# Kernel optimization log

Hardware: AMD Instinct MI355X
Metric: run time of the kernel (lower is better)

The kernel has to match this reference:

```python
import jax, jax.numpy as jnp
from jax import lax
import numpy as np

B, T, I, H, OUT = 4096, 168, 4, 64, 12


def setup_inputs() -> dict:
    key = jax.random.key(0)
    ks = jax.random.split(key, 14)
    s = 0.05
    return {
        "x": jax.random.normal(ks[0], (B, T, I), dtype=jnp.float32),
        # LSTM layer 0 (PyTorch gate order: i, f, g, o)
        "Wih0": jax.random.normal(ks[1], (4 * H, I), dtype=jnp.float32) * s,
        "Whh0": jax.random.normal(ks[2], (4 * H, H), dtype=jnp.float32) * s,
        "bih0": jax.random.normal(ks[3], (4 * H,), dtype=jnp.float32) * s,
        "bhh0": jax.random.normal(ks[4], (4 * H,), dtype=jnp.float32) * s,
        # LSTM layer 1
        "Wih1": jax.random.normal(ks[5], (4 * H, H), dtype=jnp.float32) * s,
        "Whh1": jax.random.normal(ks[6], (4 * H, H), dtype=jnp.float32) * s,
        "bih1": jax.random.normal(ks[7], (4 * H,), dtype=jnp.float32) * s,
        "bhh1": jax.random.normal(ks[8], (4 * H,), dtype=jnp.float32) * s,
        # FC head: Linear(64,64) -> ReLU -> Linear(64,12)
        "W1": jax.random.normal(ks[9], (64, H), dtype=jnp.float32) * s,
        "b1": jax.random.normal(ks[10], (64,), dtype=jnp.float32) * s,
        "W2": jax.random.normal(ks[11], (OUT, 64), dtype=jnp.float32) * s,
        "b2": jax.random.normal(ks[12], (OUT,), dtype=jnp.float32) * s,
    }


def _lstm_layer(x, Wih, Whh, bih, bhh):
    # x: [B, T, in]; returns hidden sequence [B, T, H]
    Bsz = x.shape[0]
    Hd = Whh.shape[1]
    # Precompute input contribution for all timesteps: [B, T, 4H]
    xg = jnp.einsum('bti,gi->btg', x, Wih) + bih + bhh

    def step(carry, xg_t):
        h, c = carry
        g = xg_t + h @ Whh.T  # [B, 4H]
        i, f, gg, o = jnp.split(g, 4, axis=-1)
        i = jax.nn.sigmoid(i)
        f = jax.nn.sigmoid(f)
        gg = jnp.tanh(gg)
        o = jax.nn.sigmoid(o)
        c = f * c + i * gg
        h = o * jnp.tanh(c)
        return (h, c), h

    h0 = jnp.zeros((Bsz, Hd), x.dtype)
    (_, _), hs = lax.scan(step, (h0, h0), jnp.swapaxes(xg, 0, 1))  # hs: [T, B, H]
    return jnp.swapaxes(hs, 0, 1)


def reference(x, Wih0, Whh0, bih0, bhh0, Wih1, Whh1, bih1, bhh1, W1, b1, W2, b2):
    # Eval-mode forward: dropout layers are identity.
    h1 = _lstm_layer(x, Wih0, Whh0, bih0, bhh0)   # [B, T, H]
    h2 = _lstm_layer(h1, Wih1, Whh1, bih1, bhh1)  # [B, T, H]
    last = h2[:, -1, :]                            # [B, H]
    z = jax.nn.relu(last @ W1.T + b1)              # [B, 64]
    out = z @ W2.T + b2                            # [B, 12]
    return out.reshape(-1, 3, 4)
```

## Files before the change

kernel.cpp:

```cpp
#include <hip/hip_runtime.h>


typedef _Float16 h8 __attribute__((ext_vector_type(8)));
typedef _Float16 h4 __attribute__((ext_vector_type(4)));
typedef float f4 __attribute__((ext_vector_type(4)));

#define ROWB 208
#define HBUF (16 * ROWB)
#define H0_OFF 0
#define H1_OFF (2 * HBUF)
#define SMEM_TOTAL (4 * HBUF)

__device__ __forceinline__ float rcp_(float x) {
#if __has_builtin(__builtin_amdgcn_rcpf)
  return __builtin_amdgcn_rcpf(x);
#else
  return 1.f / x;
#endif
}
__device__ __forceinline__ float sigm(float x) { return rcp_(1.f + __expf(-x)); }
__device__ __forceinline__ float tanh_(float x) { return 2.f * rcp_(1.f + __expf(-2.f * x)) - 1.f; }

__device__ __forceinline__ f4 mfma16(h8 a, h8 b, f4 c) {
  return __builtin_amdgcn_mfma_f32_16x16x32_f16(a, b, c, 0, 0, 0);
}

__device__ __forceinline__ h8 load_w8(const float* __restrict__ p) {
  h8 r;
#pragma unroll
  for (int j = 0; j < 8; j++) r[j] = (_Float16)p[j];
  return r;
}

extern "C" __global__ void __launch_bounds__(512, 2)
weather_lstm_mfma(const float* __restrict__ x,
                  const float* __restrict__ Wih0, const float* __restrict__ Whh0,
                  const float* __restrict__ bih0, const float* __restrict__ bhh0,
                  const float* __restrict__ Wih1, const float* __restrict__ Whh1,
                  const float* __restrict__ bih1, const float* __restrict__ bhh1,
                  const float* __restrict__ W1, const float* __restrict__ b1,
                  const float* __restrict__ W2, const float* __restrict__ b2,
                  float* __restrict__ out)
{
  __shared__ __align__(16) unsigned char smem[SMEM_TOTAL];
  const int tid  = threadIdx.x;
  const int lane = tid & 63;
  const int w    = tid >> 6;
  const int col  = lane & 15;
  const int quad = lane >> 4;
  const int sB   = blockIdx.x * 16;

  const int g_  = col & 3;
  const int ul_ = col >> 2;
  int arow[2];
  arow[0] = g_ * 64 + w * 8 + 0 + ul_;
  arow[1] = g_ * 64 + w * 8 + 4 + ul_;

  h8 a0[2][3];
  h8 a1i[2][2];
  h8 a1h[2][2];
#pragma unroll
  for (int T = 0; T < 2; T++) {
    const int r = arow[T];
#pragma unroll
    for (int f = 0; f < 2; f++) {
      a0[T][f]  = load_w8(Whh0 + r * 64 + f * 32 + quad * 8);
      a1i[T][f] = load_w8(Wih1 + r * 64 + f * 32 + quad * 8);
      a1h[T][f] = load_w8(Whh1 + r * 64 + f * 32 + quad * 8);
    }
    h8 xw = {};
    if (quad == 0) {
#pragma unroll
      for (int j = 0; j < 4; j++) xw[j] = (_Float16)Wih0[r * 4 + j];
    }
    a0[T][2] = xw;
  }

  f4 bias0v[2], bias1v[2];
#pragma unroll
  for (int T = 0; T < 2; T++) {
#pragma unroll
    for (int reg = 0; reg < 4; reg++) {
      const int rr = reg * 64 + w * 8 + T * 4 + quad;
      bias0v[T][reg] = bih0[rr] + bhh0[rr];
      bias1v[T][reg] = bih1[rr] + bhh1[rr];
    }
  }

  for (int idx = tid; idx < SMEM_TOTAL / 4; idx += 512) ((int*)smem)[idx] = 0;
  __syncthreads();
  if (tid < 16) {
    f4 xv = *(const f4*)(x + ((size_t)(sB + tid) * 168 + 0) * 4);
    h4 xh;
#pragma unroll
    for (int j = 0; j < 4; j++) xh[j] = (_Float16)xv[j];
    *(h4*)(smem + H0_OFF + 0 * HBUF + tid * ROWB + 128) = xh;
  }
  __syncthreads();

  float c0[2] = {0.f, 0.f}, c1[2] = {0.f, 0.f};
  float hl[2] = {0.f, 0.f};
  const int bo = col * ROWB + quad * 16;

  for (int t = 0; t < 168; t++) {
    const int pb = t & 1, nb = pb ^ 1;
    unsigned char* h0p = smem + H0_OFF + pb * HBUF;
    unsigned char* h0n = smem + H0_OFF + nb * HBUF;
    unsigned char* h1p = smem + H1_OFF + pb * HBUF;
    unsigned char* h1n = smem + H1_OFF + nb * HBUF;

    if (tid < 16) {
      const int tn = (t < 167) ? t + 1 : 167;
      f4 xv = *(const f4*)(x + ((size_t)(sB + tid) * 168 + tn) * 4);
      h4 xh;
#pragma unroll
      for (int j = 0; j < 4; j++) xh[j] = (_Float16)xv[j];
      *(h4*)(h0n + tid * ROWB + 128) = xh;
    }

    h8 b0 = *(const h8*)(h0p + bo);
    h8 b1v = *(const h8*)(h0p + bo + 64);
    h8 b2v = *(const h8*)(h0p + bo + 128);

    f4 acc0 = bias0v[0], acc1 = bias0v[1];
    acc0 = mfma16(a0[0][0], b0, acc0);
    acc1 = mfma16(a0[1][0], b0, acc1);
    acc0 = mfma16(a0[0][1], b1v, acc0);
    acc1 = mfma16(a0[1][1], b1v, acc1);
    acc0 = mfma16(a0[0][2], b2v, acc0);
    acc1 = mfma16(a0[1][2], b2v, acc1);

#pragma unroll
    for (int T = 0; T < 2; T++) {
      f4 a = T ? acc1 : acc0;
      float iv = sigm(a[0]);
      float fv = sigm(a[1]);
      float gv = tanh_(a[2]);
      float ov = sigm(a[3]);
      c0[T] = fv * c0[T] + iv * gv;
      float hn = ov * tanh_(c0[T]);
      *(_Float16*)(h0n + col * ROWB + (w * 8 + T * 4 + quad) * 2) = (_Float16)hn;
    }
    __syncthreads();

    h8 p0 = *(const h8*)(h0n + bo);
    h8 p1 = *(const h8*)(h0n + bo + 64);
    h8 q0 = *(const h8*)(h1p + bo);
    h8 q1 = *(const h8*)(h1p + bo + 64);

    acc0 = bias1v[0]; acc1 = bias1v[1];
    acc0 = mfma16(a1i[0][0], p0, acc0);
    acc1 = mfma16(a1i[1][0], p0, acc1);
    acc0 = mfma16(a1i[0][1], p1, acc0);
    acc1 = mfma16(a1i[1][1], p1, acc1);
    acc0 = mfma16(a1h[0][0], q0, acc0);
    acc1 = mfma16(a1h[1][0], q0, acc1);
    acc0 = mfma16(a1h[0][1], q1, acc0);
    acc1 = mfma16(a1h[1][1], q1, acc1);

#pragma unroll
    for (int T = 0; T < 2; T++) {
      f4 a = T ? acc1 : acc0;
      float iv = sigm(a[0]);
      float fv = sigm(a[1]);
      float gv = tanh_(a[2]);
      float ov = sigm(a[3]);
      c1[T] = fv * c1[T] + iv * gv;
      float hn = ov * tanh_(c1[T]);
      hl[T] = hn;
      *(_Float16*)(h1n + col * ROWB + (w * 8 + T * 4 + quad) * 2) = (_Float16)hn;
    }
    __syncthreads();
  }

  float* fh = (float*)smem;
#pragma unroll
  for (int T = 0; T < 2; T++)
    fh[col * 64 + (w * 8 + T * 4 + quad)] = hl[T];
  __syncthreads();

  {
    const int u = tid & 63, grp = tid >> 6;
    float za0 = b1[u], za1 = b1[u];
    const float* w1r = W1 + u * 64;
    const float* f0 = fh + (grp * 2 + 0) * 64;
    const float* f1 = fh + (grp * 2 + 1) * 64;
    for (int j = 0; j < 64; j++) {
      float wv = w1r[j];
      za0 += wv * f0[j];
      za1 += wv * f1[j];
    }
    float* zl = (float*)(smem + 4096);
    zl[(grp * 2 + 0) * 64 + u] = fmaxf(za0, 0.f);
    zl[(grp * 2 + 1) * 64 + u] = fmaxf(za1, 0.f);
  }
  __syncthreads();

  if (tid < 192) {
    const float* zl = (const float*)(smem + 4096);
    const int s = tid / 12, o = tid - s * 12;
    float a = b2[o];
    for (int j = 0; j < 64; j++) a += W2[o * 64 + j] * zl[s * 64 + j];
    out[(sB + s) * 12 + o] = a;
  }
}

extern "C" void kernel_launch(void* const* d_in, const int* in_sizes, int n_in,
                              void* d_out, int out_size, void* d_ws, size_t ws_size,
                              hipStream_t stream) {
  (void)in_sizes; (void)n_in; (void)d_ws; (void)ws_size; (void)out_size;
  const float* x    = (const float*)d_in[0];
  const float* Wih0 = (const float*)d_in[1];
  const float* Whh0 = (const float*)d_in[2];
  const float* bih0 = (const float*)d_in[3];
  const float* bhh0 = (const float*)d_in[4];
  const float* Wih1 = (const float*)d_in[5];
  const float* Whh1 = (const float*)d_in[6];
  const float* bih1 = (const float*)d_in[7];
  const float* bhh1 = (const float*)d_in[8];
  const float* W1   = (const float*)d_in[9];
  const float* b1   = (const float*)d_in[10];
  const float* W2   = (const float*)d_in[11];
  const float* b2   = (const float*)d_in[12];

  weather_lstm_mfma<<<dim3(256), dim3(512), 0, stream>>>(
      x, Wih0, Whh0, bih0, bhh0, Wih1, Whh1, bih1, bhh1, W1, b1, W2, b2,
      (float*)d_out);
}
```

Measured before the change: 252.6 us.

## Prescale gate weights by log2e, hoist layer-1 recurrent MFMAs, pack h stores

Folds the log2(e) and 2·log2(e) factors into the fp16 weights and biases so the sigmoid and tanh use raw exp2 and rcp with no per-element multiply. The layer-1 recurrent MFMAs on h1(t-1) are moved ahead of the barrier so they run alongside layer 0, shortening the serial dependency chain each timestep. Gate rows are permuted so each lane owns two adjacent hidden units, letting the two fp16 h values be written as one packed 32-bit LDS store. Scaling weights before fp16 conversion slightly changes rounding.

Result: faster. 233.3 us (-7.7%).

```diff
diff --git a/kernel.cpp b/kernel.cpp
--- a/kernel.cpp
+++ b/kernel.cpp
@@ -11,36 +11,52 @@
 #define H1_OFF (2 * HBUF)
 #define SMEM_TOTAL (4 * HBUF)
 
+#define K1F 1.4426950408889634f
+#define K2F 2.8853900817779268f
+
+__device__ __forceinline__ float exp2_(float x) {
+#if __has_builtin(__builtin_amdgcn_exp2f)
+  return __builtin_amdgcn_exp2f(x);
+#else
+  float r; asm("v_exp_f32 %0, %1" : "=v"(r) : "v"(x)); return r;
+#endif
+}
 __device__ __forceinline__ float rcp_(float x) {
 #if __has_builtin(__builtin_amdgcn_rcpf)
   return __builtin_amdgcn_rcpf(x);
 #else
-  return 1.f / x;
+  float r; asm("v_rcp_f32 %0, %1" : "=v"(r) : "v"(x)); return r;
 #endif
 }
-__device__ __forceinline__ float sigm(float x) { return rcp_(1.f + __expf(-x)); }
-__device__ __forceinline__ float tanh_(float x) { return 2.f * rcp_(1.f + __expf(-2.f * x)) - 1.f; }
+__device__ __forceinline__ float sigmp(float a) { return rcp_(1.f + exp2_(-a)); }
+__device__ __forceinline__ float tanhp(float a) { return 1.f - 2.f * rcp_(exp2_(a) + 1.f); }
 
 __device__ __forceinline__ f4 mfma16(h8 a, h8 b, f4 c) {
   return __builtin_amdgcn_mfma_f32_16x16x32_f16(a, b, c, 0, 0, 0);
 }
 
-__device__ __forceinline__ h8 load_w8(const float* __restrict__ p) {
+__device__ __forceinline__ h8 load_w8s(const float* __restrict__ p, float sc) {
   h8 r;
 #pragma unroll
-  for (int j = 0; j < 8; j++) r[j] = (_Float16)p[j];
+  for (int j = 0; j < 8; j++) r[j] = (_Float16)(p[j] * sc);
   return r;
 }
 
+__device__ __forceinline__ unsigned packh2(float a, float b) {
+  unsigned lo = (unsigned)__builtin_bit_cast(unsigned short, (_Float16)a);
+  unsigned hi = (unsigned)__builtin_bit_cast(unsigned short, (_Float16)b);
+  return lo | (hi << 16);
+}
+
 extern "C" __global__ void __launch_bounds__(512, 2)
-weather_lstm_mfma(const float* __restrict__ x,
-                  const float* __restrict__ Wih0, const float* __restrict__ Whh0,
-                  const float* __restrict__ bih0, const float* __restrict__ bhh0,
-                  const float* __restrict__ Wih1, const float* __restrict__ Whh1,
-                  const float* __restrict__ bih1, const float* __restrict__ bhh1,
-                  const float* __restrict__ W1, const float* __restrict__ b1,
-                  const float* __restrict__ W2, const float* __restrict__ b2,
-                  float* __restrict__ out)
+weather_lstm_mfma3(const float* __restrict__ x,
+                   const float* __restrict__ Wih0, const float* __restrict__ Whh0,
+                   const float* __restrict__ bih0, const float* __restrict__ bhh0,
+                   const float* __restrict__ Wih1, const float* __restrict__ Whh1,
+                   const float* __restrict__ bih1, const float* __restrict__ bhh1,
+                   const float* __restrict__ W1, const float* __restrict__ b1,
+                   const float* __restrict__ W2, const float* __restrict__ b2,
+                   float* __restrict__ out)
 {
   __shared__ __align__(16) unsigned char smem[SMEM_TOTAL];
   const int tid  = threadIdx.x;
@@ -52,26 +68,25 @@
 
   const int g_  = col & 3;
   const int ul_ = col >> 2;
+  const float asc = (g_ == 2) ? K2F : K1F;
   int arow[2];
-  arow[0] = g_ * 64 + w * 8 + 0 + ul_;
-  arow[1] = g_ * 64 + w * 8 + 4 + ul_;
-
-  h8 a0[2][3];
-  h8 a1i[2][2];
-  h8 a1h[2][2];
+  arow[0] = g_ * 64 + w * 8 + 2 * ul_ + 0;
+  arow[1] = g_ * 64 + w * 8 + 2 * ul_ + 1;
+
+  h8 a0[2][3], a1i[2][2], a1h[2][2];
 #pragma unroll
   for (int T = 0; T < 2; T++) {
     const int r = arow[T];
 #pragma unroll
     for (int f = 0; f < 2; f++) {
-      a0[T][f]  = load_w8(Whh0 + r * 64 + f * 32 + quad * 8);
-      a1i[T][f] = load_w8(Wih1 + r * 64 + f * 32 + quad * 8);
-      a1h[T][f] = load_w8(Whh1 + r * 64 + f * 32 + quad * 8);
+      a0[T][f]  = load_w8s(Whh0 + r * 64 + f * 32 + quad * 8, asc);
+      a1i[T][f] = load_w8s(Wih1 + r * 64 + f * 32 + quad * 8, asc);
+      a1h[T][f] = load_w8s(Whh1 + r * 64 + f * 32 + quad * 8, asc);
     }
     h8 xw = {};
     if (quad == 0) {
 #pragma unroll
-      for (int j = 0; j < 4; j++) xw[j] = (_Float16)Wih0[r * 4 + j];
+      for (int j = 0; j < 4; j++) xw[j] = (_Float16)(Wih0[r * 4 + j] * asc);
     }
     a0[T][2] = xw;
   }
@@ -81,9 +96,10 @@
   for (int T = 0; T < 2; T++) {
 #pragma unroll
     for (int reg = 0; reg < 4; reg++) {
-      const int rr = reg * 64 + w * 8 + T * 4 + quad;
-      bias0v[T][reg] = bih0[rr] + bhh0[rr];
-      bias1v[T][reg] = bih1[rr] + bhh1[rr];
+      const int rr = reg * 64 + w * 8 + 2 * quad + T;
+      const float bs = (reg == 2) ? K2F : K1F;
+      bias0v[T][reg] = (bih0[rr] + bhh0[rr]) * bs;
+      bias1v[T][reg] = (bih1[rr] + bhh1[rr]) * bs;
     }
   }
 
@@ -101,6 +117,7 @@
   float c0[2] = {0.f, 0.f}, c1[2] = {0.f, 0.f};
   float hl[2] = {0.f, 0.f};
   const int bo = col * ROWB + quad * 16;
+  const int wo = col * ROWB + (w * 8 + 2 * quad) * 2;
 
   for (int t = 0; t < 168; t++) {
     const int pb = t & 1, nb = pb ^ 1;
@@ -118,65 +135,63 @@
       *(h4*)(h0n + tid * ROWB + 128) = xh;
     }
 
-    h8 b0 = *(const h8*)(h0p + bo);
+    h8 b0  = *(const h8*)(h0p + bo);
     h8 b1v = *(const h8*)(h0p + bo + 64);
     h8 b2v = *(const h8*)(h0p + bo + 128);
-
-    f4 acc0 = bias0v[0], acc1 = bias0v[1];
-    acc0 = mfma16(a0[0][0], b0, acc0);
-    acc1 = mfma16(a0[1][0], b0, acc1);
+    h8 q0  = *(const h8*)(h1p + bo);
+    h8 q1  = *(const h8*)(h1p + bo + 64);
+
+    f4 l1a0 = mfma16(a1h[0][0], q0, bias1v[0]);
+    f4 l1a1 = mfma16(a1h[1][0], q0, bias1v[1]);
+    l1a0 = mfma16(a1h[0][1], q1, l1a0);
+    l1a1 = mfma16(a1h[1][1], q1, l1a1);
+
+    f4 acc0 = mfma16(a0[0][0], b0, bias0v[0]);
+    f4 acc1 = mfma16(a0[1][0], b0, bias0v[1]);
     acc0 = mfma16(a0[0][1], b1v, acc0);
     acc1 = mfma16(a0[1][1], b1v, acc1);
     acc0 = mfma16(a0[0][2], b2v, acc0);
     acc1 = mfma16(a0[1][2], b2v, acc1);
 
+    float h0o[2];
 #pragma unroll
     for (int T = 0; T < 2; T++) {
       f4 a = T ? acc1 : acc0;
-      float iv = sigm(a[0]);
-      float fv = sigm(a[1]);
-      float gv = tanh_(a[2]);
-      float ov = sigm(a[3]);
+      float iv = sigmp(a[0]);
+      float fv = sigmp(a[1]);
+      float gv = tanhp(a[2]);
+      float ov = sigmp(a[3]);
       c0[T] = fv * c0[T] + iv * gv;
-      float hn = ov * tanh_(c0[T]);
-      *(_Float16*)(h0n + col * ROWB + (w * 8 + T * 4 + quad) * 2) = (_Float16)hn;
-    }
+      h0o[T] = ov * tanhp(c0[T] * K2F);
+    }
+    *(unsigned*)(h0n + wo) = packh2(h0o[0], h0o[1]);
     __syncthreads();
 
     h8 p0 = *(const h8*)(h0n + bo);
     h8 p1 = *(const h8*)(h0n + bo + 64);
-    h8 q0 = *(const h8*)(h1p + bo);
-    h8 q1 = *(const h8*)(h1p + bo + 64);
-
-    acc0 = bias1v[0]; acc1 = bias1v[1];
-    acc0 = mfma16(a1i[0][0], p0, acc0);
-    acc1 = mfma16(a1i[1][0], p0, acc1);
-    acc0 = mfma16(a1i[0][1], p1, acc0);
-    acc1 = mfma16(a1i[1][1], p1, acc1);
-    acc0 = mfma16(a1h[0][0], q0, acc0);
-    acc1 = mfma16(a1h[1][0], q0, acc1);
-    acc0 = mfma16(a1h[0][1], q1, acc0);
-    acc1 = mfma16(a1h[1][1], q1, acc1);
+    l1a0 = mfma16(a1i[0][0], p0, l1a0);
+    l1a1 = mfma16(a1i[1][0], p0, l1a1);
+    l1a0 = mfma16(a1i[0][1], p1, l1a0);
+    l1a1 = mfma16(a1i[1][1], p1, l1a1);
 
 #pragma unroll
     for (int T = 0; T < 2; T++) {
-      f4 a = T ? acc1 : acc0;
-      float iv = sigm(a[0]);
-      float fv = sigm(a[1]);
-      float gv = tanh_(a[2]);
-      float ov = sigm(a[3]);
+      f4 a = T ? l1a1 : l1a0;
+      float iv = sigmp(a[0]);
+      float fv = sigmp(a[1]);
+      float gv = tanhp(a[2]);
+      float ov = sigmp(a[3]);
       c1[T] = fv * c1[T] + iv * gv;
-      float hn = ov * tanh_(c1[T]);
-      hl[T] = hn;
-      *(_Float16*)(h1n + col * ROWB + (w * 8 + T * 4 + quad) * 2) = (_Float16)hn;
-    }
+      hl[T] = ov * tanhp(c1[T] * K2F);
+    }
+    *(unsigned*)(h1n + wo) = packh2(hl[0], hl[1]);
     __syncthreads();
   }
 
   float* fh = (float*)smem;
 #pragma unroll
   for (int T = 0; T < 2; T++)
-    fh[col * 64 + (w * 8 + T * 4 + quad)] = hl[T];
+    fh[col * 64 + (w * 8 + 2 * quad + T)] = hl[T];
   __syncthreads();
 
   {
@@ -223,7 +238,7 @@
   const float* W2   = (const float*)d_in[11];
   const float* b2   = (const float*)d_in[12];
 
-  weather_lstm_mfma<<<dim3(256), dim3(512), 0, stream>>>(
+  weather_lstm_mfma3<<<dim3(256), dim3(512), 0, stream>>>(
       x, Wih0, Whh0, bih0, bhh0, Wih1, Whh1, bih1, bhh1, W1, b1, W2, b2,
       (float*)d_out);
 }
```
